# Kernel tuning notes

Hardware: AMD Instinct MI355X
Metric: run time of the kernel (lower is better)

Reference implementation:

```python
import jax, jax.numpy as jnp
import numpy as np

N_NODES, N_EDGES = 50000, 800000
IN_CH, HID, HEADS, OUT_CH = 128, 64, 4, 2
NEG_SLOPE = 0.2
EPS = 1e-16


def setup_inputs() -> dict:
    key = jax.random.key(0)
    ks = jax.random.split(key, 16)
    def rn(k, shape, scale=0.1):
        return jax.random.normal(k, shape, dtype=jnp.float32) * scale
    inp = {
        "x": jax.random.normal(ks[0], (N_NODES, IN_CH), dtype=jnp.float32),
        "edge_index": jax.random.randint(ks[1], (2, N_EDGES), 0, N_NODES, dtype=jnp.int64),
        "stats": jax.random.normal(ks[2], (N_EDGES, 3), dtype=jnp.float32),
        # conv1: GATConv(IN_CH -> HID, heads=HEADS, concat=True)
        "W1": rn(ks[3], (IN_CH, HEADS * HID)),
        "att_src1": rn(ks[4], (HEADS, HID)),
        "att_dst1": rn(ks[5], (HEADS, HID)),
        "b1": rn(ks[6], (HEADS * HID,)),
        # conv2: GATConv(HEADS*HID -> HID, heads=1, concat=False)
        "W2": rn(ks[7], (HEADS * HID, HID)),
        "att_src2": rn(ks[8], (1, HID)),
        "att_dst2": rn(ks[9], (1, HID)),
        "b2": rn(ks[10], (HID,)),
        # edge MLP: Linear(2*HID+3 -> HID) -> ReLU -> Linear(HID -> OUT_CH)
        "mW1": rn(ks[11], (2 * HID + 3, HID)),
        "mb1": rn(ks[12], (HID,)),
        "mW2": rn(ks[13], (HID, OUT_CH)),
        "mb2": rn(ks[14], (OUT_CH,)),
    }
    return inp


def gat_layer(x, src, dst, W, att_s, att_d, n_nodes):
    """PyG GATConv core: per-edge attention, softmax over destination, scatter-add."""
    H, C = att_s.shape
    h = (x @ W).reshape(n_nodes, H, C)                      # [N,H,C]
    a_s = jnp.sum(h * att_s, axis=-1)                        # [N,H]
    a_d = jnp.sum(h * att_d, axis=-1)                        # [N,H]
    e = a_s[src] + a_d[dst]                                  # [E,H]
    e = jnp.where(e > 0, e, NEG_SLOPE * e)                   # leaky_relu
    m = jax.ops.segment_max(e, dst, num_segments=n_nodes)    # [N,H]
    m = jnp.where(jnp.isfinite(m), m, 0.0)
    e = jnp.exp(e - m[dst])
    s = jax.ops.segment_sum(e, dst, num_segments=n_nodes)    # [N,H]
    alpha = e / (s[dst] + EPS)                               # [E,H]
    out = jax.ops.segment_sum(alpha[:, :, None] * h[src], dst, num_segments=n_nodes)
    return out                                               # [N,H,C]


def reference(x, edge_index, stats, W1, att_src1, att_dst1, b1,
              W2, att_src2, att_dst2, b2, mW1, mb1, mW2, mb2):
    n = x.shape[0]
    row, col = edge_index[0], edge_index[1]
    # add self loops (PyG GATConv default)
    loop = jnp.arange(n, dtype=edge_index.dtype)
    src = jnp.concatenate([row, loop])
    dst = jnp.concatenate([col, loop])

    # conv1: heads concatenated, then ELU (dropout disabled at inference)
    h1 = gat_layer(x, src, dst, W1, att_src1, att_dst1, n)
    h1 = h1.reshape(n, HEADS * HID) + b1
    h1 = jax.nn.elu(h1)

    # conv2: single head, concat=False (mean over 1 head == squeeze)
    h2 = gat_layer(h1, src, dst, W2, att_src2, att_dst2, n)
    node_emb = h2[:, 0, :] + b2                              # [N,HID]

    # edge MLP over gathered endpoint embeddings + per-edge stats
    feat = jnp.concatenate([node_emb[row], node_emb[col], stats], axis=1)  # [E,2*HID+3]
    hidden = jax.nn.relu(feat @ mW1 + mb1)
    return hidden @ mW2 + mb2                                # [E,OUT_CH]
```

## Files before the change

kernel.cpp:

```cpp
#include <hip/hip_runtime.h>
#include <math.h>

#define NN 50000
#define NE 800000
#define EP (NE + NN)
#define INC 128
#define HID 64
#define HEADS 4
#define C1 (HEADS * HID)
#define NEG 0.2f
#define EPSS 1e-16f

#define SCHUNK 512
#define NSB ((NN + SCHUNK - 1) / SCHUNK)

#define KP  170
#define KP1 136
#define KP2 264
typedef __attribute__((ext_vector_type(8))) short bf16x8;
typedef __attribute__((ext_vector_type(4))) float f32x4;

__device__ __forceinline__ unsigned short f2bf(float f) {
    unsigned u = __float_as_uint(f);
    unsigned r = (u + 0x7FFFu + ((u >> 16) & 1u)) >> 16;
    return (unsigned short)r;
}
__device__ __forceinline__ float bf2f(unsigned short b) {
    return __uint_as_float(((unsigned)b) << 16);
}

__global__ __launch_bounds__(SCHUNK) void scan_partial(const int* __restrict__ counts,
                                                       int* __restrict__ bsum) {
    __shared__ int lds[SCHUNK];
    int i = blockIdx.x * SCHUNK + threadIdx.x;
    lds[threadIdx.x] = (i < NN) ? counts[i] : 0;
    __syncthreads();
    for (int off = SCHUNK / 2; off > 0; off >>= 1) {
        if (threadIdx.x < off) lds[threadIdx.x] += lds[threadIdx.x + off];
        __syncthreads();
    }
    if (threadIdx.x == 0) bsum[blockIdx.x] = lds[0];
}

__global__ void scan_top(int* __restrict__ bsum, int* __restrict__ rowptr) {
    __shared__ int lds[NSB];
    int t = threadIdx.x;
    if (t < NSB) lds[t] = bsum[t];
    __syncthreads();
    if (t == 0) {
        int acc = 0;
        for (int i = 0; i < NSB; ++i) { int v = lds[i]; lds[i] = acc; acc += v; }
        rowptr[NN] = acc;
    }
    __syncthreads();
    if (t < NSB) bsum[t] = lds[t];
}

__global__ __launch_bounds__(SCHUNK) void scan_final(const int* __restrict__ counts,
                                                     const int* __restrict__ bsum,
                                                     int* __restrict__ rowptr,
                                                     int* __restrict__ cursor) {
    __shared__ int lds[SCHUNK];
    int i = blockIdx.x * SCHUNK + threadIdx.x;
    int v = (i < NN) ? counts[i] : 0;
    lds[threadIdx.x] = v;
    __syncthreads();
    for (int off = 1; off < SCHUNK; off <<= 1) {
        int t = (threadIdx.x >= off) ? lds[threadIdx.x - off] : 0;
        __syncthreads();
        lds[threadIdx.x] += t;
        __syncthreads();
    }
    if (i < NN) {
        int excl = lds[threadIdx.x] - v + bsum[blockIdx.x];
        rowptr[i] = excl;
        cursor[i] = excl;
    }
}

__global__ void csr_fill(const int* __restrict__ ei, int* __restrict__ cursor,
                         int* __restrict__ csr_src, int* __restrict__ csr_dst) {
    int e = blockIdx.x * 256 + threadIdx.x;
    if (e >= EP) return;
    int s, d;
    if (e < NE) { s = ei[e]; d = ei[NE + e]; } else { s = d = e - NE; }
    int pos = atomicAdd(&cursor[d], 1);
    csr_src[pos] = s;
    csr_dst[pos] = d;
}

#define PREP_N0 (64 * KP)
#define PREP_N1 (C1 * INC)
#define PREP_N2 (HID * C1)
#define PREP_TOT (PREP_N0 + PREP_N1 + PREP_N2)
__global__ void prep_all(const float* __restrict__ mW1, const float* __restrict__ W1,
                         const float* __restrict__ W2, const int* __restrict__ ei,
                         unsigned short* __restrict__ wTh, unsigned short* __restrict__ wTl,
                         unsigned short* __restrict__ w1h, unsigned short* __restrict__ w1l,
                         unsigned short* __restrict__ w2h, unsigned short* __restrict__ w2l,
                         int* __restrict__ counts) {
    int i = blockIdx.x * 256 + threadIdx.x;
    if (i < PREP_N0) {
        int c = i / KP, k = i % KP;
        unsigned short h = 0, l = 0;
        if (k < 131) {
            float f = mW1[k * 64 + c];
            h = f2bf(f);
            l = f2bf(f - bf2f(h));
        }
        wTh[i] = h; wTl[i] = l;
        return;
    }
    i -= PREP_N0;
    if (i < PREP_N1) {
        int c = i >> 7, k = i & 127;
        float f = W1[k * C1 + c];
        unsigned short h = f2bf(f);
        w1h[i] = h; w1l[i] = f2bf(f - bf2f(h));
        return;
    }
    i -= PREP_N1;
    if (i < PREP_N2) {
        int c = i >> 8, k = i & 255;
        float f = W2[k * HID + c];
        unsigned short h = f2bf(f);
        w2h[i] = h; w2l[i] = f2bf(f - bf2f(h));
        return;
    }
    i -= PREP_N2;
    if (i < EP) {
        int d = (i < NE) ? ei[NE + i] : (i - NE);
        atomicAdd(&counts[d], 1);
    }
}

__global__ void edge_w1k(const int* __restrict__ csr_src, const int* __restrict__ csr_dst,
                         const float* __restrict__ as1, const float* __restrict__ ad1,
                         float* __restrict__ w1e) {
    int i = blockIdx.x * 256 + threadIdx.x;
    if (i >= EP) return;
    int s = csr_src[i], d = csr_dst[i];
    float4 a = *(const float4*)(as1 + s * 4);
    float4 b = *(const float4*)(ad1 + d * 4);
    float4 o;
    float t;
    t = a.x + b.x; t = t > 0.f ? t : NEG * t; o.x = __expf(t);
    t = a.y + b.y; t = t > 0.f ? t : NEG * t; o.y = __expf(t);
    t = a.z + b.z; t = t > 0.f ? t : NEG * t; o.z = __expf(t);
    t = a.w + b.w; t = t > 0.f ? t : NEG * t; o.w = __expf(t);
    *(float4*)(w1e + (size_t)i * 4) = o;
}

__global__ void edge_w2k(const int* __restrict__ csr_src, const int* __restrict__ csr_dst,
                         const float* __restrict__ as2, const float* __restrict__ ad2,
                         float* __restrict__ w2e) {
    int i = blockIdx.x * 256 + threadIdx.x;
    if (i >= EP) return;
    float t = as2[csr_src[i]] + ad2[csr_dst[i]];
    t = t > 0.f ? t : NEG * t;
    w2e[i] = __expf(t);
}

__global__ __launch_bounds__(256) void gemm1_mfma(const float* __restrict__ x,
                                                  const unsigned short* __restrict__ w1h,
                                                  const unsigned short* __restrict__ w1l,
                                                  const float* __restrict__ att_s,
                                                  const float* __restrict__ att_d,
                                                  unsigned short* __restrict__ h1b,
                                                  float* __restrict__ as1,
                                                  float* __restrict__ ad1) {
    __shared__ unsigned short wH[64 * KP1];
    __shared__ unsigned short wL[64 * KP1];
    const int tid = threadIdx.x;
    const int n0 = blockIdx.x * 64;
    const int q  = blockIdx.y;

    for (int idx = tid; idx < 64 * 16; idx += 256) {
        int col = idx >> 4, ch = idx & 15;
        *(bf16x8*)(wH + col * KP1 + ch * 8) =
            *(const bf16x8*)(w1h + ((q * 64 + col) << 7) + ch * 8);
        *(bf16x8*)(wL + col * KP1 + ch * 8) =
            *(const bf16x8*)(w1l + ((q * 64 + col) << 7) + ch * 8);
    }

    const int w = tid >> 6, l = tid & 63;
    const int cl = l & 15, g = l >> 4, g8 = g * 8;
    const int na = min(n0 + w * 16 + cl, NN - 1);

    bf16x8 aH[4], aL[4];
#pragma unroll
    for (int kk = 0; kk < 4; ++kk) {
        const float* ap = x + (size_t)na * INC + kk * 32 + g8;
        float4 v0 = *(const float4*)ap;
        float4 v1 = *(const float4*)(ap + 4);
        float vv[8] = {v0.x, v0.y, v0.z, v0.w, v1.x, v1.y, v1.z, v1.w};
#pragma unroll
        for (int j = 0; j < 8; ++j) {
            unsigned short h = f2bf(vv[j]);
            aH[kk][j] = (short)h;
            aL[kk][j] = (short)f2bf(vv[j] - bf2f(h));
        }
    }

    f32x4 acc[4];
#pragma unroll
    for (int ct = 0; ct < 4; ++ct) acc[ct] = (f32x4){0.f, 0.f, 0.f, 0.f};

    __syncthreads();

#pragma unroll
    for (int kk = 0; kk < 4; ++kk) {
        const int ko = kk * 32 + g8;
#pragma unroll
        for (int ct = 0; ct < 4; ++ct) {
            const bf16x8 bH = *(const bf16x8*)(wH + (ct * 16 + cl) * KP1 + ko);
            const bf16x8 bL = *(const bf16x8*)(wL + (ct * 16 + cl) * KP1 + ko);
            acc[ct] = __builtin_amdgcn_mfma_f32_16x16x32_bf16(aH[kk], bH, acc[ct], 0, 0, 0);
            acc[ct] = __builtin_amdgcn_mfma_f32_16x16x32_bf16(aH[kk], bL, acc[ct], 0, 0, 0);
            acc[ct] = __builtin_amdgcn_mfma_f32_16x16x32_bf16(aL[kk], bH, acc[ct], 0, 0, 0);
        }
    }

    float asc[4], adc[4];
#pragma unroll
    for (int ct = 0; ct < 4; ++ct) {
        asc[ct] = att_s[q * 64 + ct * 16 + cl];
        adc[ct] = att_d[q * 64 + ct * 16 + cl];
    }

#pragma unroll
    for (int reg = 0; reg < 4; ++reg) {
        const int nd = n0 + w * 16 + g * 4 + reg;
        float sa = 0.f, sd = 0.f;
#pragma unroll
        for (int ct = 0; ct < 4; ++ct) {
            sa += acc[ct][reg] * asc[ct];
            sd += acc[ct][reg] * adc[ct];
        }
#pragma unroll
        for (int off = 8; off > 0; off >>= 1) {
            sa += __shfl_xor(sa, off);
            sd += __shfl_xor(sd, off);
        }
        if (nd < NN) {
#pragma unroll
            for (int ct = 0; ct < 4; ++ct)
                h1b[(size_t)nd * C1 + q * 64 + ct * 16 + cl] = f2bf(acc[ct][reg]);
            if (cl == 0) { as1[nd * 4 + q] = sa; ad1[nd * 4 + q] = sd; }
        }
    }
}

__global__ __launch_bounds__(256) void gemm2_mfma(const unsigned short* __restrict__ h1c,
                                                  const unsigned short* __restrict__ w2h,
                                                  const unsigned short* __restrict__ w2l,
                                                  const float* __restrict__ att_s,
                                                  const float* __restrict__ att_d,
                                                  unsigned short* __restrict__ h2b,
                                                  float* __restrict__ as2,
                                                  float* __restrict__ ad2) {
    __shared__ unsigned short wH[64 * KP2];
    __shared__ unsigned short wL[64 * KP2];
    const int tid = threadIdx.x;
    const int n0 = blockIdx.x * 64;

    for (int idx = tid; idx < 64 * 32; idx += 256) {
        int col = idx >> 5, ch = idx & 31;
        *(bf16x8*)(wH + col * KP2 + ch * 8) =
            *(const bf16x8*)(w2h + ((col) << 8) + ch * 8);
        *(bf16x8*)(wL + col * KP2 + ch * 8) =
            *(const bf16x8*)(w2l + ((col) << 8) + ch * 8);
    }

    const int w = tid >> 6, l = tid & 63;
    const int cl = l & 15, g = l >> 4, g8 = g * 8;
    const int na = min(n0 + w * 16 + cl, NN - 1);

    f32x4 acc[4];
#pragma unroll
    for (int ct = 0; ct < 4; ++ct) acc[ct] = (f32x4){0.f, 0.f, 0.f, 0.f};

    __syncthreads();

#pragma unroll
    for (int kk = 0; kk < 8; ++kk) {
        const bf16x8 aH = *(const bf16x8*)(h1c + (size_t)na * C1 + kk * 32 + g8);
        const int ko = kk * 32 + g8;
#pragma unroll
        for (int ct = 0; ct < 4; ++ct) {
            const bf16x8 bH = *(const bf16x8*)(wH + (ct * 16 + cl) * KP2 + ko);
            const bf16x8 bL = *(const bf16x8*)(wL + (ct * 16 + cl) * KP2 + ko);
            acc[ct] = __builtin_amdgcn_mfma_f32_16x16x32_bf16(aH, bH, acc[ct], 0, 0, 0);
            acc[ct] = __builtin_amdgcn_mfma_f32_16x16x32_bf16(aH, bL, acc[ct], 0, 0, 0);
        }
    }

    float asc[4], adc[4];
#pragma unroll
    for (int ct = 0; ct < 4; ++ct) {
        asc[ct] = att_s[ct * 16 + cl];
        adc[ct] = att_d[ct * 16 + cl];
    }

#pragma unroll
    for (int reg = 0; reg < 4; ++reg) {
        const int nd = n0 + w * 16 + g * 4 + reg;
        float sa = 0.f, sd = 0.f;
#pragma unroll
        for (int ct = 0; ct < 4; ++ct) {
            sa += acc[ct][reg] * asc[ct];
            sd += acc[ct][reg] * adc[ct];
        }
#pragma unroll
        for (int off = 8; off > 0; off >>= 1) {
            sa += __shfl_xor(sa, off);
            sd += __shfl_xor(sd, off);
        }
        if (nd < NN) {
#pragma unroll
            for (int ct = 0; ct < 4; ++ct)
                h2b[(size_t)nd * HID + ct * 16 + cl] = f2bf(acc[ct][reg]);
            if (cl == 0) { as2[nd] = sa; ad2[nd] = sd; }
        }
    }
}

__global__ __launch_bounds__(256) void conv1_agg(const int* __restrict__ rowptr,
                                                 const int* __restrict__ csr_src,
                                                 const float* __restrict__ w1e,
                                                 const unsigned short* __restrict__ h1b,
                                                 const float* __restrict__ b1,
                                                 unsigned short* __restrict__ h1c) {
    const int tid  = threadIdx.x;
    const int wid  = tid >> 6;
    const int l    = tid & 63;
    const int half = l >> 5;
    const int l32  = l & 31;
    const int node = blockIdx.x * 8 + wid * 2 + half;
    const int hd   = l32 >> 3;
    const int beg = rowptr[node], end = rowptr[node + 1];

    float acc[8] = {0.f, 0.f, 0.f, 0.f, 0.f, 0.f, 0.f, 0.f};
    float sm = 0.f;
#pragma unroll 2
    for (int i = beg; i < end; ++i) {
        int s = csr_src[i];
        float w = w1e[(size_t)i * 4 + hd];
        bf16x8 hv = *(const bf16x8*)(h1b + (size_t)s * C1 + l32 * 8);
#pragma unroll
        for (int j = 0; j < 8; ++j)
            acc[j] += w * bf2f((unsigned short)hv[j]);
        sm += w;
    }
    const float rden = 1.f / (sm + EPSS);

    const float* bp = b1 + l32 * 8;
    bf16x8 ob;
#pragma unroll
    for (int j = 0; j < 8; ++j) {
        float o = acc[j] * rden + bp[j];
        o = o > 0.f ? o : (__expf(o) - 1.f);
        ob[j] = (short)f2bf(o);
    }
    *(bf16x8*)(h1c + (size_t)node * C1 + l32 * 8) = ob;
}

__global__ __launch_bounds__(256) void conv2_agg(const int* __restrict__ rowptr,
                                                 const int* __restrict__ csr_src,
                                                 const float* __restrict__ w2e,
                                                 const unsigned short* __restrict__ h2b,
                                                 const float* __restrict__ b2,
                                                 unsigned short* __restrict__ embb) {
    const int tid  = threadIdx.x;
    const int wid  = tid >> 6;
    const int l    = tid & 63;
    const int half = l >> 5;
    const int l32  = l & 31;
    const int node = blockIdx.x * 8 + wid * 2 + half;
    const int beg = rowptr[node], end = rowptr[node + 1];

    float a0 = 0.f, a1 = 0.f, sm = 0.f;
#pragma unroll 2
    for (int i = beg; i < end; ++i) {
        int s = csr_src[i];
        float w = w2e[i];
        unsigned hv = *(const unsigned*)(h2b + (size_t)s * HID + l32 * 2);
        a0 += w * bf2f((unsigned short)(hv & 0xFFFF));
        a1 += w * bf2f((unsigned short)(hv >> 16));
        sm += w;
    }
    const float rden = 1.f / (sm + EPSS);
    float o0 = a0 * rden + b2[l32 * 2];
    float o1 = a1 * rden + b2[l32 * 2 + 1];
    unsigned outw = (unsigned)f2bf(o0) | ((unsigned)f2bf(o1) << 16);
    *(unsigned*)(embb + (size_t)node * HID + l32 * 2) = outw;
}

__global__ __launch_bounds__(256) void edge_mlp_mfma(const int* __restrict__ ei,
                                                     const unsigned short* __restrict__ embb,
                                                     const float* __restrict__ stats,
                                                     const unsigned short* __restrict__ wTh,
                                                     const unsigned short* __restrict__ wTl,
                                                     const float* __restrict__ mb1,
                                                     const float* __restrict__ mW2,
                                                     const float* __restrict__ mb2,
                                                     float* __restrict__ out) {
    const int l  = threadIdx.x & 63;
    const int cl = l & 15;
    const int g  = l >> 4;
    const int g8 = g * 8;

    bf16x8 bH[5][4], bL[5][4];
#pragma unroll
    for (int kk = 0; kk < 5; ++kk)
#pragma unroll
        for (int ct = 0; ct < 4; ++ct) {
            bH[kk][ct] = *(const bf16x8*)(wTh + (ct * 16 + cl) * KP + kk * 32 + g8);
            bL[kk][ct] = *(const bf16x8*)(wTl + (ct * 16 + cl) * KP + kk * 32 + g8);
        }

    float bia[4], w2a[4], w2b[4];
#pragma unroll
    for (int ct = 0; ct < 4; ++ct) {
        bia[ct] = mb1[ct * 16 + cl];
        w2a[ct] = mW2[(ct * 16 + cl) * 2 + 0];
        w2b[ct] = mW2[(ct * 16 + cl) * 2 + 1];
    }
    const float ob0 = mb2[0], ob1 = mb2[1];

    const int wave0  = blockIdx.x * 4 + (threadIdx.x >> 6);
    const int nwaves = gridDim.x * 4;

    for (int t = wave0; t < NE / 16; t += nwaves) {
        const int ge_a = t * 16 + cl;
        const int rn = ei[ge_a];
        const int cn = ei[NE + ge_a];
        const unsigned short* rp = embb + (size_t)rn * HID;
        const unsigned short* cp = embb + (size_t)cn * HID;

        bf16x8 aH[5];
        aH[0] = *(const bf16x8*)(rp + g8);
        aH[1] = *(const bf16x8*)(rp + 32 + g8);
        aH[2] = *(const bf16x8*)(cp + g8);
        aH[3] = *(const bf16x8*)(cp + 32 + g8);
        {
            bf16x8 z = {0, 0, 0, 0, 0, 0, 0, 0};
            if (g == 0) {
                z[0] = (short)f2bf(stats[(size_t)ge_a * 3 + 0]);
                z[1] = (short)f2bf(stats[(size_t)ge_a * 3 + 1]);
                z[2] = (short)f2bf(stats[(size_t)ge_a * 3 + 2]);
            }
            aH[4] = z;
        }

        f32x4 acc[4];
#pragma unroll
        for (int ct = 0; ct < 4; ++ct)
            acc[ct] = (f32x4){bia[ct], bia[ct], bia[ct], bia[ct]};

#pragma unroll
        for (int kk = 0; kk < 5; ++kk) {
#pragma unroll
            for (int ct = 0; ct < 4; ++ct) {
                acc[ct] = __builtin_amdgcn_mfma_f32_16x16x32_bf16(aH[kk], bH[kk][ct], acc[ct], 0, 0, 0);
                acc[ct] = __builtin_amdgcn_mfma_f32_16x16x32_bf16(aH[kk], bL[kk][ct], acc[ct], 0, 0, 0);
            }
        }

#pragma unroll
        for (int reg = 0; reg < 4; ++reg) {
            float p0 = 0.f, p1 = 0.f;
#pragma unroll
            for (int ct = 0; ct < 4; ++ct) {
                float h = fmaxf(acc[ct][reg], 0.f);
                p0 += h * w2a[ct];
                p1 += h * w2b[ct];
            }
#pragma unroll
            for (int off = 8; off > 0; off >>= 1) {
                p0 += __shfl_xor(p0, off);
                p1 += __shfl_xor(p1, off);
            }
            if (cl == 0) {
                const int ge = t * 16 + g * 4 + reg;
                *(float2*)(out + (size_t)ge * 2) = make_float2(p0 + ob0, p1 + ob1);
            }
        }
    }
}

extern "C" void kernel_launch(void* const* d_in, const int* in_sizes, int n_in,
                              void* d_out, int out_size, void* d_ws, size_t ws_size,
                              hipStream_t stream) {
    const float* x      = (const float*)d_in[0];
    const int*   ei     = (const int*)d_in[1];
    const float* stats  = (const float*)d_in[2];
    const float* W1     = (const float*)d_in[3];
    const float* att_s1 = (const float*)d_in[4];
    const float* att_d1 = (const float*)d_in[5];
    const float* b1     = (const float*)d_in[6];
    const float* W2     = (const float*)d_in[7];
    const float* att_s2 = (const float*)d_in[8];
    const float* att_d2 = (const float*)d_in[9];
    const float* b2     = (const float*)d_in[10];
    const float* mW1    = (const float*)d_in[11];
    const float* mb1    = (const float*)d_in[12];
    const float* mW2    = (const float*)d_in[13];
    const float* mb2    = (const float*)d_in[14];
    float* out = (float*)d_out;
    float* ws  = (float*)d_ws;

    int*   rowptr  = (int*)ws;
    int*   csr_src = rowptr + NN + 16;
    int*   csr_dst = csr_src + EP;
    float* as1     = (float*)(csr_dst + EP);
    float* ad1     = as1 + (size_t)4 * NN;
    unsigned short* h1b = (unsigned short*)(ad1 + (size_t)4 * NN);
    unsigned short* h1c = h1b + (size_t)256 * NN;
    unsigned short* h2b = h1c + (size_t)256 * NN;
    unsigned short* embb = h2b + (size_t)64 * NN;
    float* as2     = (float*)(embb + (size_t)64 * NN);
    float* ad2     = as2 + NN;
    unsigned short* wTh = (unsigned short*)(ad2 + NN);
    unsigned short* wTl = wTh + 64 * KP;
    unsigned short* w1h = wTl + 64 * KP;
    unsigned short* w1l = w1h + C1 * INC;
    unsigned short* w2h = w1l + C1 * INC;
    unsigned short* w2l = w2h + HID * C1;
    float* w1e     = (float*)(w2l + HID * C1 + 64);
    float* w2e     = w1e + (size_t)4 * EP;
    int*   counts  = (int*)(w2e + EP + 64);
    int*   bsum    = counts + NN + 64;
    int*   cursor  = bsum + NSB + 64;

    hipMemsetAsync(counts, 0, NN * sizeof(int), stream);
    prep_all<<<(PREP_TOT + EP + 255) / 256, 256, 0, stream>>>(
        mW1, W1, W2, ei, wTh, wTl, w1h, w1l, w2h, w2l, counts);
    scan_partial<<<NSB, SCHUNK, 0, stream>>>(counts, bsum);
    scan_top<<<1, 128, 0, stream>>>(bsum, rowptr);
    scan_final<<<NSB, SCHUNK, 0, stream>>>(counts, bsum, rowptr, cursor);
    csr_fill<<<(EP + 255) / 256, 256, 0, stream>>>(ei, cursor, csr_src, csr_dst);

    gemm1_mfma<<<dim3((NN + 63) / 64, 4), 256, 0, stream>>>(x, w1h, w1l, att_s1, att_d1,
                                                            h1b, as1, ad1);
    edge_w1k<<<(EP + 255) / 256, 256, 0, stream>>>(csr_src, csr_dst, as1, ad1, w1e);
    conv1_agg<<<NN / 8, 256, 0, stream>>>(rowptr, csr_src, w1e, h1b, b1, h1c);

    gemm2_mfma<<<(NN + 63) / 64, 256, 0, stream>>>(h1c, w2h, w2l, att_s2, att_d2,
                                                   h2b, as2, ad2);
    edge_w2k<<<(EP + 255) / 256, 256, 0, stream>>>(csr_src, csr_dst, as2, ad2, w2e);
    conv2_agg<<<NN / 8, 256, 0, stream>>>(rowptr, csr_src, w2e, h2b, b2, embb);

    edge_mlp_mfma<<<512, 256, 0, stream>>>(ei, embb, stats, wTh, wTl,
                                           mb1, mW2, mb2, out);
}
```

Baseline: 319.3 us.

## Prefetch next edge tile in edge MLP and apply stats term in fp32

The edge MLP kernel now loads the next tile's endpoint embeddings and stats into registers before running the current tile's MFMAs, a software-pipelined gather meant to hide global-memory latency. The fifth K-slice, which only held three stats values padded to 32, is dropped. Those three stats terms are instead added as fp32 FMAs after the MFMA, removing 8 MFMAs per tile and the bf16 rounding of stats. Register pressure goes up from the double-buffered inputs, and the launch bound now asks for 2 blocks per CU.

```diff
diff --git a/kernel.cpp b/kernel.cpp
--- a/kernel.cpp
+++ b/kernel.cpp
@@ -396,61 +396,94 @@
     *(unsigned*)(embb + (size_t)node * HID + l32 * 2) = outw;
 }
 
-__global__ __launch_bounds__(256) void edge_mlp_mfma(const int* __restrict__ ei,
-                                                     const unsigned short* __restrict__ embb,
-                                                     const float* __restrict__ stats,
-                                                     const unsigned short* __restrict__ wTh,
-                                                     const unsigned short* __restrict__ wTl,
-                                                     const float* __restrict__ mb1,
-                                                     const float* __restrict__ mW2,
-                                                     const float* __restrict__ mb2,
-                                                     float* __restrict__ out) {
+__global__ __launch_bounds__(256, 2) void edge_mlp_mfma(const int* __restrict__ ei,
+                                                        const unsigned short* __restrict__ embb,
+                                                        const float* __restrict__ stats,
+                                                        const unsigned short* __restrict__ wTh,
+                                                        const unsigned short* __restrict__ wTl,
+                                                        const float* __restrict__ mW1,
+                                                        const float* __restrict__ mb1,
+                                                        const float* __restrict__ mW2,
+                                                        const float* __restrict__ mb2,
+                                                        float* __restrict__ out) {
     const int l  = threadIdx.x & 63;
     const int cl = l & 15;
     const int g  = l >> 4;
     const int g8 = g * 8;
 
-    bf16x8 bH[5][4], bL[5][4];
-#pragma unroll
-    for (int kk = 0; kk < 5; ++kk)
+    bf16x8 bH[4][4], bL[4][4];
+#pragma unroll
+    for (int kk = 0; kk < 4; ++kk)
 #pragma unroll
         for (int ct = 0; ct < 4; ++ct) {
             bH[kk][ct] = *(const bf16x8*)(wTh + (ct * 16 + cl) * KP + kk * 32 + g8);
             bL[kk][ct] = *(const bf16x8*)(wTl + (ct * 16 + cl) * KP + kk * 32 + g8);
         }
 
+    float w1s0[4], w1s1[4], w1s2[4];
     float bia[4], w2a[4], w2b[4];
 #pragma unroll
     for (int ct = 0; ct < 4; ++ct) {
-        bia[ct] = mb1[ct * 16 + cl];
-        w2a[ct] = mW2[(ct * 16 + cl) * 2 + 0];
-        w2b[ct] = mW2[(ct * 16 + cl) * 2 + 1];
+        const int col = ct * 16 + cl;
+        w1s0[ct] = mW1[128 * 64 + col];
+        w1s1[ct] = mW1[129 * 64 + col];
+        w1s2[ct] = mW1[130 * 64 + col];
+        bia[ct] = mb1[col];
+        w2a[ct] = mW2[col * 2 + 0];
+        w2b[ct] = mW2[col * 2 + 1];
     }
     const float ob0 = mb2[0], ob1 = mb2[1];
 
     const int wave0  = blockIdx.x * 4 + (threadIdx.x >> 6);
     const int nwaves = gridDim.x * 4;
-
-    for (int t = wave0; t < NE / 16; t += nwaves) {
-        const int ge_a = t * 16 + cl;
-        const int rn = ei[ge_a];
-        const int cn = ei[NE + ge_a];
+    const int NT = NE / 16;
+
+    int t = wave0;
+    if (t >= NT) return;
+
+    bf16x8 a0, a1, a2, a3;
+    float st[12];
+    {
+        const int rn = ei[t * 16 + cl];
+        const int cn = ei[NE + t * 16 + cl];
         const unsigned short* rp = embb + (size_t)rn * HID;
         const unsigned short* cp = embb + (size_t)cn * HID;
-
-        bf16x8 aH[5];
-        aH[0] = *(const bf16x8*)(rp + g8);
-        aH[1] = *(const bf16x8*)(rp + 32 + g8);
-        aH[2] = *(const bf16x8*)(cp + g8);
-        aH[3] = *(const bf16x8*)(cp + 32 + g8);
-        {
-            bf16x8 z = {0, 0, 0, 0, 0, 0, 0, 0};
-            if (g == 0) {
-                z[0] = (short)f2bf(stats[(size_t)ge_a * 3 + 0]);
-                z[1] = (short)f2bf(stats[(size_t)ge_a * 3 + 1]);
-                z[2] = (short)f2bf(stats[(size_t)ge_a * 3 + 2]);
+        a0 = *(const bf16x8*)(rp + g8);
+        a1 = *(const bf16x8*)(rp + 32 + g8);
+        a2 = *(const bf16x8*)(cp + g8);
+        a3 = *(const bf16x8*)(cp + 32 + g8);
+#pragma unroll
+        for (int r = 0; r < 4; ++r) {
+            const size_t e = (size_t)(t * 16 + g * 4 + r) * 3;
+            st[r * 3 + 0] = stats[e + 0];
+            st[r * 3 + 1] = stats[e + 1];
+            st[r * 3 + 2] = stats[e + 2];
+        }
+    }
+
+    while (t < NT) {
+        const int tn = t + nwaves;
+        bf16x8 c0 = a0, c1 = a1, c2 = a2, c3 = a3;
+        float cst[12];
+#pragma unroll
+        for (int j = 0; j < 12; ++j) cst[j] = st[j];
+
+        if (tn < NT) {
+            const int rn = ei[tn * 16 + cl];
+            const int cn = ei[NE + tn * 16 + cl];
+            const unsigned short* rp = embb + (size_t)rn * HID;
+            const unsigned short* cp = embb + (size_t)cn * HID;
+            a0 = *(const bf16x8*)(rp + g8);
+            a1 = *(const bf16x8*)(rp + 32 + g8);
+            a2 = *(const bf16x8*)(cp + g8);
+            a3 = *(const bf16x8*)(cp + 32 + g8);
+#pragma unroll
+            for (int r = 0; r < 4; ++r) {
+                const size_t e = (size_t)(tn * 16 + g * 4 + r) * 3;
+                st[r * 3 + 0] = stats[e + 0];
+                st[r * 3 + 1] = stats[e + 1];
+                st[r * 3 + 2] = stats[e + 2];
             }
-            aH[4] = z;
         }
 
         f32x4 acc[4];
@@ -459,12 +492,15 @@
             acc[ct] = (f32x4){bia[ct], bia[ct], bia[ct], bia[ct]};
 
 #pragma unroll
-        for (int kk = 0; kk < 5; ++kk) {
-#pragma unroll
-            for (int ct = 0; ct < 4; ++ct) {
-                acc[ct] = __builtin_amdgcn_mfma_f32_16x16x32_bf16(aH[kk], bH[kk][ct], acc[ct], 0, 0, 0);
-                acc[ct] = __builtin_amdgcn_mfma_f32_16x16x32_bf16(aH[kk], bL[kk][ct], acc[ct], 0, 0, 0);
-            }
+        for (int ct = 0; ct < 4; ++ct) {
+            acc[ct] = __builtin_amdgcn_mfma_f32_16x16x32_bf16(c0, bH[0][ct], acc[ct], 0, 0, 0);
+            acc[ct] = __builtin_amdgcn_mfma_f32_16x16x32_bf16(c0, bL[0][ct], acc[ct], 0, 0, 0);
+            acc[ct] = __builtin_amdgcn_mfma_f32_16x16x32_bf16(c1, bH[1][ct], acc[ct], 0, 0, 0);
+            acc[ct] = __builtin_amdgcn_mfma_f32_16x16x32_bf16(c1, bL[1][ct], acc[ct], 0, 0, 0);
+            acc[ct] = __builtin_amdgcn_mfma_f32_16x16x32_bf16(c2, bH[2][ct], acc[ct], 0, 0, 0);
+            acc[ct] = __builtin_amdgcn_mfma_f32_16x16x32_bf16(c2, bL[2][ct], acc[ct], 0, 0, 0);
+            acc[ct] = __builtin_amdgcn_mfma_f32_16x16x32_bf16(c3, bH[3][ct], acc[ct], 0, 0, 0);
+            acc[ct] = __builtin_amdgcn_mfma_f32_16x16x32_bf16(c3, bL[3][ct], acc[ct], 0, 0, 0);
         }
 
 #pragma unroll
@@ -472,7 +508,11 @@
             float p0 = 0.f, p1 = 0.f;
 #pragma unroll
             for (int ct = 0; ct < 4; ++ct) {
-                float h = fmaxf(acc[ct][reg], 0.f);
+                float h = acc[ct][reg]
+                        + cst[reg * 3 + 0] * w1s0[ct]
+                        + cst[reg * 3 + 1] * w1s1[ct]
+                        + cst[reg * 3 + 2] * w1s2[ct];
+                h = fmaxf(h, 0.f);
                 p0 += h * w2a[ct];
                 p1 += h * w2b[ct];
             }
@@ -486,6 +526,7 @@
                 *(float2*)(out + (size_t)ge * 2) = make_float2(p0 + ob0, p1 + ob1);
             }
         }
+        t = tn;
     }
 }
 
@@ -551,6 +592,6 @@
     edge_w2k<<<(EP + 255) / 256, 256, 0, stream>>>(csr_src, csr_dst, as2, ad2, w2e);
     conv2_agg<<<NN / 8, 256, 0, stream>>>(rowptr, csr_src, w2e, h2b, b2, embb);
 
-    edge_mlp_mfma<<<512, 256, 0, stream>>>(ei, embb, stats, wTh, wTl,
+    edge_mlp_mfma<<<512, 256, 0, stream>>>(ei, embb, stats, wTh, wTl, mW1,
                                            mb1, mW2, mb2, out);
 }
```

After: 311.0 us. 1.03x faster.

## Restructure edge MLP: 64 edges per wave, fragment-layout weights, fp32 stats epilogue

Applied to the files above, without the earlier changes.

The edge MLP kernel now has each wave handle 64 edges (four 16-edge tiles) with one launch per tile group instead of a persistent grid-stride loop. It loads B fragments from a prepacked, fragment-ordered weight buffer inside the K loop, so each fragment is reused across four tiles instead of being held in registers for the whole kernel. The three stats columns are removed from the MFMA K dimension and added as fp32 FMAs in the epilogue, which drops one K step of MFMAs and the bf16 rounding of stats. It also reads stats with vector loads. Register pressure rises from the 4x4 accumulators, and the change depends on NE being divisible by 256.

```diff
diff --git a/kernel.cpp b/kernel.cpp
--- a/kernel.cpp
+++ b/kernel.cpp
@@ -14,7 +14,6 @@
 #define SCHUNK 512
 #define NSB ((NN + SCHUNK - 1) / SCHUNK)
 
-#define KP  170
 #define KP1 136
 #define KP2 264
 typedef __attribute__((ext_vector_type(8))) short bf16x8;
@@ -89,42 +88,45 @@
     csr_dst[pos] = d;
 }
 
-#define PREP_N0 (64 * KP)
-#define PREP_N1 (C1 * INC)
-#define PREP_N2 (HID * C1)
+#define PREP_N0 (C1 * INC)
+#define PREP_N1 (HID * C1)
+#define PREP_N2 (4 * 4 * 64 * 8)
 #define PREP_TOT (PREP_N0 + PREP_N1 + PREP_N2)
 __global__ void prep_all(const float* __restrict__ mW1, const float* __restrict__ W1,
                          const float* __restrict__ W2, const int* __restrict__ ei,
-                         unsigned short* __restrict__ wTh, unsigned short* __restrict__ wTl,
                          unsigned short* __restrict__ w1h, unsigned short* __restrict__ w1l,
                          unsigned short* __restrict__ w2h, unsigned short* __restrict__ w2l,
+                         unsigned short* __restrict__ wFh, unsigned short* __restrict__ wFl,
                          int* __restrict__ counts) {
     int i = blockIdx.x * 256 + threadIdx.x;
     if (i < PREP_N0) {
-        int c = i / KP, k = i % KP;
-        unsigned short h = 0, l = 0;
-        if (k < 131) {
-            float f = mW1[k * 64 + c];
-            h = f2bf(f);
-            l = f2bf(f - bf2f(h));
-        }
-        wTh[i] = h; wTl[i] = l;
-        return;
-    }
-    i -= PREP_N0;
-    if (i < PREP_N1) {
         int c = i >> 7, k = i & 127;
         float f = W1[k * C1 + c];
         unsigned short h = f2bf(f);
         w1h[i] = h; w1l[i] = f2bf(f - bf2f(h));
         return;
     }
-    i -= PREP_N1;
-    if (i < PREP_N2) {
+    i -= PREP_N0;
+    if (i < PREP_N1) {
         int c = i >> 8, k = i & 255;
         float f = W2[k * HID + c];
         unsigned short h = f2bf(f);
         w2h[i] = h; w2l[i] = f2bf(f - bf2f(h));
+        return;
+    }
+    i -= PREP_N1;
+    if (i < PREP_N2) {
+        int kk = i >> 11;
+        int ct = (i >> 9) & 3;
+        int l  = (i >> 3) & 63;
+        int j  = i & 7;
+        int cl = l & 15, g = l >> 4;
+        int k   = kk * 32 + g * 8 + j;
+        int col = ct * 16 + cl;
+        float f = mW1[k * 64 + col];
+        unsigned short h = f2bf(f);
+        wFh[i] = h;
+        wFl[i] = f2bf(f - bf2f(h));
         return;
     }
     i -= PREP_N2;
@@ -396,83 +398,90 @@
     *(unsigned*)(embb + (size_t)node * HID + l32 * 2) = outw;
 }
 
-__global__ __launch_bounds__(256) void edge_mlp_mfma(const int* __restrict__ ei,
-                                                     const unsigned short* __restrict__ embb,
-                                                     const float* __restrict__ stats,
-                                                     const unsigned short* __restrict__ wTh,
-                                                     const unsigned short* __restrict__ wTl,
-                                                     const float* __restrict__ mb1,
-                                                     const float* __restrict__ mW2,
-                                                     const float* __restrict__ mb2,
-                                                     float* __restrict__ out) {
+__global__ __launch_bounds__(256, 2) void edge_mlp_mfma(const int* __restrict__ ei,
+                                                        const unsigned short* __restrict__ embb,
+                                                        const float* __restrict__ stats,
+                                                        const unsigned short* __restrict__ wFh,
+                                                        const unsigned short* __restrict__ wFl,
+                                                        const float* __restrict__ mW1,
+                                                        const float* __restrict__ mb1,
+                                                        const float* __restrict__ mW2,
+                                                        const float* __restrict__ mb2,
+                                                        float* __restrict__ out) {
     const int l  = threadIdx.x & 63;
     const int cl = l & 15;
     const int g  = l >> 4;
     const int g8 = g * 8;
 
-    bf16x8 bH[5][4], bL[5][4];
-#pragma unroll
-    for (int kk = 0; kk < 5; ++kk)
-#pragma unroll
-        for (int ct = 0; ct < 4; ++ct) {
-            bH[kk][ct] = *(const bf16x8*)(wTh + (ct * 16 + cl) * KP + kk * 32 + g8);
-            bL[kk][ct] = *(const bf16x8*)(wTl + (ct * 16 + cl) * KP + kk * 32 + g8);
-        }
-
-    float bia[4], w2a[4], w2b[4];
+    float w1s0[4], w1s1[4], w1s2[4], bia[4], w2a[4], w2b[4];
 #pragma unroll
     for (int ct = 0; ct < 4; ++ct) {
-        bia[ct] = mb1[ct * 16 + cl];
-        w2a[ct] = mW2[(ct * 16 + cl) * 2 + 0];
-        w2b[ct] = mW2[(ct * 16 + cl) * 2 + 1];
+        const int col = ct * 16 + cl;
+        w1s0[ct] = mW1[128 * 64 + col];
+        w1s1[ct] = mW1[129 * 64 + col];
+        w1s2[ct] = mW1[130 * 64 + col];
+        bia[ct] = mb1[col];
+        w2a[ct] = mW2[col * 2 + 0];
+        w2b[ct] = mW2[col * 2 + 1];
     }
     const float ob0 = mb2[0], ob1 = mb2[1];
 
-    const int wave0  = blockIdx.x * 4 + (threadIdx.x >> 6);
-    const int nwaves = gridDim.x * 4;
-
-    for (int t = wave0; t < NE / 16; t += nwaves) {
-        const int ge_a = t * 16 + cl;
+    const int t = blockIdx.x * 4 + (threadIdx.x >> 6);
+
+    bf16x8 a[4][4];
+#pragma unroll
+    for (int s = 0; s < 4; ++s) {
+        const int ge_a = t * 64 + s * 16 + cl;
         const int rn = ei[ge_a];
         const int cn = ei[NE + ge_a];
         const unsigned short* rp = embb + (size_t)rn * HID;
         const unsigned short* cp = embb + (size_t)cn * HID;
-
-        bf16x8 aH[5];
-        aH[0] = *(const bf16x8*)(rp + g8);
-        aH[1] = *(const bf16x8*)(rp + 32 + g8);
-        aH[2] = *(const bf16x8*)(cp + g8);
-        aH[3] = *(const bf16x8*)(cp + 32 + g8);
-        {
-            bf16x8 z = {0, 0, 0, 0, 0, 0, 0, 0};
-            if (g == 0) {
-                z[0] = (short)f2bf(stats[(size_t)ge_a * 3 + 0]);
-                z[1] = (short)f2bf(stats[(size_t)ge_a * 3 + 1]);
-                z[2] = (short)f2bf(stats[(size_t)ge_a * 3 + 2]);
+        a[s][0] = *(const bf16x8*)(rp + g8);
+        a[s][1] = *(const bf16x8*)(rp + 32 + g8);
+        a[s][2] = *(const bf16x8*)(cp + g8);
+        a[s][3] = *(const bf16x8*)(cp + 32 + g8);
+    }
+
+    f32x4 acc[4][4];
+#pragma unroll
+    for (int s = 0; s < 4; ++s)
+#pragma unroll
+        for (int ct = 0; ct < 4; ++ct)
+            acc[s][ct] = (f32x4){bia[ct], bia[ct], bia[ct], bia[ct]};
+
+#pragma unroll
+    for (int kk = 0; kk < 4; ++kk) {
+#pragma unroll
+        for (int ct = 0; ct < 4; ++ct) {
+            const int fo = ((kk * 4 + ct) * 64 + l) * 8;
+            const bf16x8 bH = *(const bf16x8*)(wFh + fo);
+            const bf16x8 bL = *(const bf16x8*)(wFl + fo);
+#pragma unroll
+            for (int s = 0; s < 4; ++s) {
+                acc[s][ct] = __builtin_amdgcn_mfma_f32_16x16x32_bf16(a[s][kk], bH, acc[s][ct], 0, 0, 0);
+                acc[s][ct] = __builtin_amdgcn_mfma_f32_16x16x32_bf16(a[s][kk], bL, acc[s][ct], 0, 0, 0);
             }
-            aH[4] = z;
-        }
-
-        f32x4 acc[4];
-#pragma unroll
-        for (int ct = 0; ct < 4; ++ct)
-            acc[ct] = (f32x4){bia[ct], bia[ct], bia[ct], bia[ct]};
-
-#pragma unroll
-        for (int kk = 0; kk < 5; ++kk) {
-#pragma unroll
-            for (int ct = 0; ct < 4; ++ct) {
-                acc[ct] = __builtin_amdgcn_mfma_f32_16x16x32_bf16(aH[kk], bH[kk][ct], acc[ct], 0, 0, 0);
-                acc[ct] = __builtin_amdgcn_mfma_f32_16x16x32_bf16(aH[kk], bL[kk][ct], acc[ct], 0, 0, 0);
-            }
-        }
-
+        }
+    }
+
+#pragma unroll
+    for (int s = 0; s < 4; ++s) {
+        const float* sp = stats + (size_t)(t * 64 + s * 16 + g * 4) * 3;
+        float4 s0 = *(const float4*)(sp);
+        float4 s1 = *(const float4*)(sp + 4);
+        float4 s2 = *(const float4*)(sp + 8);
+        float cst[12] = {s0.x, s0.y, s0.z, s0.w, s1.x, s1.y, s1.z, s1.w,
+                         s2.x, s2.y, s2.z, s2.w};
 #pragma unroll
         for (int reg = 0; reg < 4; ++reg) {
             float p0 = 0.f, p1 = 0.f;
 #pragma unroll
             for (int ct = 0; ct < 4; ++ct) {
-                float h = fmaxf(acc[ct][reg], 0.f);
+                float h = acc[s][ct][reg]
+                        + cst[reg * 3 + 0] * w1s0[ct]
+                        + cst[reg * 3 + 1] * w1s1[ct]
+                        + cst[reg * 3 + 2] * w1s2[ct];
+                h = fmaxf(h, 0.f);
                 p0 += h * w2a[ct];
                 p1 += h * w2b[ct];
             }
@@ -482,7 +491,7 @@
                 p1 += __shfl_xor(p1, off);
             }
             if (cl == 0) {
-                const int ge = t * 16 + g * 4 + reg;
+                const int ge = t * 64 + s * 16 + g * 4 + reg;
                 *(float2*)(out + (size_t)ge * 2) = make_float2(p0 + ob0, p1 + ob1);
             }
         }
@@ -521,13 +530,13 @@
     unsigned short* embb = h2b + (size_t)64 * NN;
     float* as2     = (float*)(embb + (size_t)64 * NN);
     float* ad2     = as2 + NN;
-    unsigned short* wTh = (unsigned short*)(ad2 + NN);
-    unsigned short* wTl = wTh + 64 * KP;
-    unsigned short* w1h = wTl + 64 * KP;
+    unsigned short* w1h = (unsigned short*)(ad2 + NN);
     unsigned short* w1l = w1h + C1 * INC;
     unsigned short* w2h = w1l + C1 * INC;
     unsigned short* w2l = w2h + HID * C1;
-    float* w1e     = (float*)(w2l + HID * C1 + 64);
+    unsigned short* wFh = w2l + HID * C1;
+    unsigned short* wFl = wFh + PREP_N2;
+    float* w1e     = (float*)(wFl + PREP_N2 + 64);
     float* w2e     = w1e + (size_t)4 * EP;
     int*   counts  = (int*)(w2e + EP + 64);
     int*   bsum    = counts + NN + 64;
@@ -535,7 +544,7 @@
 
     hipMemsetAsync(counts, 0, NN * sizeof(int), stream);
     prep_all<<<(PREP_TOT + EP + 255) / 256, 256, 0, stream>>>(
-        mW1, W1, W2, ei, wTh, wTl, w1h, w1l, w2h, w2l, counts);
+        mW1, W1, W2, ei, w1h, w1l, w2h, w2l, wFh, wFl, counts);
     scan_partial<<<NSB, SCHUNK, 0, stream>>>(counts, bsum);
     scan_top<<<1, 128, 0, stream>>>(bsum, rowptr);
     scan_final<<<NSB, SCHUNK, 0, stream>>>(counts, bsum, rowptr, cursor);
@@ -551,6 +560,6 @@
     edge_w2k<<<(EP + 255) / 256, 256, 0, stream>>>(csr_src, csr_dst, as2, ad2, w2e);
     conv2_agg<<<NN / 8, 256, 0, stream>>>(rowptr, csr_src, w2e, h2b, b2, embb);
 
-    edge_mlp_mfma<<<512, 256, 0, stream>>>(ei, embb, stats, wTh, wTl,
-                                           mb1, mW2, mb2, out);
-}
+    edge_mlp_mfma<<<(NE / 64) / 4, 256, 0, stream>>>(ei, embb, stats, wFh, wFl, mW1,
+                                                     mb1, mW2, mb2, out);
+}
```

New measurement: 318.4 us. No clear change (-0.3%).
